# Kernel tuning notes

Measured on AMD Instinct MI355X. Metric: run time of the kernel, lower is better.

The kernel has to match this reference:

```python
import jax, jax.numpy as jnp
import numpy as np

B, N, K, C_IN, D = 4, 2048, 16, 480, 64
EPS = 1e-5


def _c1(x, w, b):
    # 1x1 Conv1d: x (B,C,N), w (O,C) -> (B,O,N)
    return jnp.einsum('oc,bcn->bon', w, x) + b[:, None]


def _c2(x, w, b):
    # 1x1 Conv2d: x (B,C,J,N), w (O,C) -> (B,O,J,N)
    return jnp.einsum('oc,bcjn->bojn', w, x) + b[:, None, None]


def _bn(x, g, b):
    # eval-mode BatchNorm2d with running_mean=0, running_var=1
    return x * (g / jnp.sqrt(1.0 + EPS))[:, None, None] + b[:, None, None]


def _mlp_res(x, w1, b1, w2, b2, ws, bs):
    return _c1(jax.nn.relu(_c1(x, w1, b1)), w2, b2) + _c1(x, ws, bs)


def _group(f, idx):
    # f (B,C,N), idx (B,K,N) int -> out[b,c,j,n] = f[b,c,idx[b,j,n]]  -> (B,C,K,N)
    return jax.vmap(lambda ff, ii: ff[:, ii])(f, idx)


def _knn_idx(xyz):
    # xyz (B,3,N) -> idx (B,K,N), excluding the self point (nearest neighbor)
    pts = xyz.transpose(0, 2, 1)  # (B,N,3)
    sq = jnp.sum(pts * pts, -1)
    d2 = sq[:, :, None] + sq[:, None, :] - 2.0 * jnp.einsum('bnd,bmd->bnm', pts, pts)
    _, idx = jax.lax.top_k(-d2, K + 1)  # (B,N,K+1), nearest first
    return idx.transpose(0, 2, 1)[:, 1:, :]  # drop self -> (B,K,N)


def _forward(idx, feature, xyz, bt1_w, bt1_b, bt2_w, bt2_b, bts_w, bts_b,
             q_w, q_b, k_w, k_b, v_w, v_b,
             fd1_w, fd1_b, fd_g, fd_bb, fd2_w, fd2_b,
             fg1_w, fg1_b, fg_g, fg_bb, fg2_w, fg2_b,
             at_w, at_b, m41_w, m41_b, m42_w, m42_b):
    x = _mlp_res(feature, bt1_w, bt1_b, bt2_w, bt2_b, bts_w, bts_b)  # (B,64,N)
    q = _c1(x, q_w, q_b)
    k = _c1(x, k_w, k_b)
    v = _c1(x, v_w, v_b)

    group_xyz = _group(xyz, idx)                       # (B,3,K,N)
    rel_xyz = xyz[:, :, None, :] - group_xyz           # (B,3,K,N)
    pos_enc = _c2(jax.nn.relu(_bn(_c2(rel_xyz, fd1_w, fd1_b), fd_g, fd_bb)), fd2_w, fd2_b)  # (B,64,K,N)

    k_local = _group(k, idx)                           # (B,64,K,N)
    v_local = _group(v, idx)
    qk_rel = q[:, :, None, :] - k_local
    attn = _c2(jax.nn.relu(_bn(_c2(qk_rel + pos_enc, fg1_w, fg1_b), fg_g, fg_bb)), fg2_w, fg2_b)  # (B,64,K,N)

    attn1 = attn.transpose(0, 1, 3, 2)                 # (B,64,N,K)
    # ConvTranspose2d(64,64,(4,1),(4,1)) with kernel==stride: out[b,o,4n+r,f] = sum_c x[b,c,n,f]*W[c,o,r] + bias[o]
    y = jnp.einsum('bcnf,cor->bonrf', attn1, at_w)
    y = y.reshape(y.shape[0], y.shape[1], -1, y.shape[4]) + at_b[None, :, None, None]  # (B,64,4N,K)
    attn = jax.nn.softmax(y, axis=1)

    value_rel = (v_local + pos_enc).transpose(0, 1, 3, 2)   # (B,64,N,K)
    value = jnp.repeat(value_rel, 4, axis=2)                # nearest upsample (4,1) -> (B,64,4N,K)

    res = jnp.einsum('bmnf,bmnf->bmn', attn, value)         # (B,64,4N)
    identity = jnp.repeat(x, 4, axis=2)                     # nearest upsample x4 -> (B,64,4N)
    res = res + identity
    completion = _c1(jax.nn.relu(_c1(res, m41_w, m41_b)), m42_w, m42_b)  # (B,3,4N)
    return completion, res


def setup_inputs() -> dict:
    key = jax.random.key(0)
    ks = jax.random.split(key, 24)
    i = iter(range(24))

    def w(shape):
        return (jax.random.normal(ks[next(i)], shape, dtype=jnp.float32) * 0.05)

    z = lambda n: jnp.zeros((n,), jnp.float32)
    o = lambda n: jnp.ones((n,), jnp.float32)
    return {
        'feature': jax.random.normal(ks[next(i)], (B, C_IN, N), dtype=jnp.float32),
        'xyz': jax.random.normal(ks[next(i)], (B, 3, N), dtype=jnp.float32),
        'bt1_w': w((D, C_IN)), 'bt1_b': z(D),
        'bt2_w': w((D, D)), 'bt2_b': z(D),
        'bts_w': w((D, C_IN)), 'bts_b': z(D),
        'q_w': w((D, D)), 'q_b': z(D),
        'k_w': w((D, D)), 'k_b': z(D),
        'v_w': w((D, D)), 'v_b': z(D),
        'fd1_w': w((D, 3)), 'fd1_b': z(D), 'fd_g': o(D), 'fd_bb': z(D),
        'fd2_w': w((D, D)), 'fd2_b': z(D),
        'fg1_w': w((4 * D, D)), 'fg1_b': z(4 * D), 'fg_g': o(4 * D), 'fg_bb': z(4 * D),
        'fg2_w': w((D, 4 * D)), 'fg2_b': z(D),
        'at_w': w((D, D, 4)), 'at_b': z(D),
        'm41_w': w((D, D)), 'm41_b': z(D),
        'm42_w': w((3, D)), 'm42_b': z(3),
    }


def reference(feature, xyz, bt1_w, bt1_b, bt2_w, bt2_b, bts_w, bts_b,
              q_w, q_b, k_w, k_b, v_w, v_b,
              fd1_w, fd1_b, fd_g, fd_bb, fd2_w, fd2_b,
              fg1_w, fg1_b, fg_g, fg_bb, fg2_w, fg2_b,
              at_w, at_b, m41_w, m41_b, m42_w, m42_b):
    idx = _knn_idx(xyz)
    return _forward(idx, feature, xyz, bt1_w, bt1_b, bt2_w, bt2_b, bts_w, bts_b,
                    q_w, q_b, k_w, k_b, v_w, v_b,
                    fd1_w, fd1_b, fd_g, fd_bb, fd2_w, fd2_b,
                    fg1_w, fg1_b, fg_g, fg_bb, fg2_w, fg2_b,
                    at_w, at_b, m41_w, m41_b, m42_w, m42_b)
```

## Files before the change

### kernel.cpp

```cpp
#include <hip/hip_runtime.h>

#define B_ 4
#define N_ 2048
#define K_ 16
#define CIN_ 480
#define UPN_ 8192
#define M_ (B_*N_*K_)
#define MX_ (B_*N_)
#define KCAP 448

typedef unsigned int u32;
typedef unsigned short u16;
typedef unsigned long long u64;
typedef __attribute__((ext_vector_type(8))) short short8;
typedef __attribute__((ext_vector_type(4))) float f32x4;

#define DEV static __device__ __forceinline__

DEV float b2f(u16 h){ return __uint_as_float(((u32)h)<<16); }
DEV u16 f2b(float f){
  u32 u = __float_as_uint(f);
  u32 r = u + 0x7fffu + ((u>>16)&1u);
  return (u16)(r>>16);
}
DEV u32 pack2(float a, float b){ return (u32)f2b(a) | ((u32)f2b(b)<<16); }
DEV bool detect_bf(const void* fg){ return ((((const u32*)fg)[0]) & 0xFFFFu) == 0x3F80u; }
DEV float ld(const void* p, int i, bool bf){
  return bf ? b2f(((const u16*)p)[i]) : ((const float*)p)[i];
}
DEV u64 makekey(float d2, int m){
  u32 bits = __float_as_uint(d2);
  bits = (bits & 0x80000000u) ? ~bits : (bits | 0x80000000u);
  return ((u64)bits<<32) | (u32)m;
}
DEV int swz64(int row, int colByte){ return row*128 + (colByte ^ ((row&7)<<4)); }
DEV int swzH (int row, int colByte){ return row*512 + (colByte ^ ((row&7)<<4)); }

__global__ __launch_bounds__(256) void convert_kernel(const void* __restrict__ xyz,
    const void* __restrict__ fg, float* __restrict__ fxyz)
{
  bool bf = detect_bf(fg);
  const int XT = B_*3*N_;
  for(int i = blockIdx.x*256+threadIdx.x; i < XT; i += gridDim.x*256)
    fxyz[i] = bf ? b2f(((const u16*)xyz)[i]) : ((const float*)xyz)[i];
}

__global__ __launch_bounds__(256) void transpose_kernel(const void* __restrict__ feature,
    const void* __restrict__ fg, u16* __restrict__ fxbT)
{
  __shared__ u16 s[32][34];
  bool bf = detect_bf(fg);
  int ntile = blockIdx.x, ctile = blockIdx.y, b = blockIdx.z;
  int tx = threadIdx.x & 31, ty = threadIdx.x >> 5;
  u64 base = (u64)b*CIN_*N_;
  #pragma unroll
  for(int r=0;r<4;r++){
    int c = ctile*32 + ty + r*8;
    int n = ntile*32 + tx;
    u64 i = base + (u64)c*N_ + n;
    s[ty + r*8][tx] = bf ? ((const u16*)feature)[i] : f2b(((const float*)feature)[i]);
  }
  __syncthreads();
  #pragma unroll
  for(int r=0;r<4;r++){
    int nl = ty + r*8;
    int n = ntile*32 + nl;
    fxbT[(u64)b*N_*CIN_ + (u64)n*CIN_ + ctile*32 + tx] = s[tx][nl];
  }
}

__global__ __launch_bounds__(256) void prep_kernel(
    const void* __restrict__ bt1_w, const void* __restrict__ bt1_b,
    const void* __restrict__ bt2_w, const void* __restrict__ bt2_b,
    const void* __restrict__ bts_w, const void* __restrict__ bts_b,
    const void* __restrict__ q_w, const void* __restrict__ q_b,
    const void* __restrict__ k_w, const void* __restrict__ k_b,
    const void* __restrict__ v_w, const void* __restrict__ v_b,
    const void* __restrict__ fd1_w, const void* __restrict__ fd1_b,
    const void* __restrict__ fd_g, const void* __restrict__ fd_bb,
    const void* __restrict__ fd2_w, const void* __restrict__ fd2_b,
    const void* __restrict__ fg1_w, const void* __restrict__ fg1_b,
    const void* __restrict__ fg_g, const void* __restrict__ fg_bb,
    const void* __restrict__ fg2_w, const void* __restrict__ fg2_b,
    const void* __restrict__ at_w, const void* __restrict__ at_b,
    const void* __restrict__ m41_w, const void* __restrict__ m41_b,
    const void* __restrict__ m42_w, const void* __restrict__ m42_b,
    float* __restrict__ W, u16* __restrict__ WB)
{
  int t = blockIdx.x*256 + threadIdx.x;
// ... 60 lines not shown
  __syncthreads();
  int w = threadIdx.x>>6, l = threadIdx.x&63;
  int q = blockIdx.x*4 + w;
  float qx=px[q], qy=py[q], qz=pz[q], qs=sq[q];
  float d2c[32];
  u64 best=~0ull;
  #pragma unroll
  for(int j=0;j<32;j++){
    int m = l*32 + ((j+l)&31);
    float d2 = (qs+sq[m]) - 2.0f*(qx*px[m]+qy*py[m]+qz*pz[m]);
    d2c[j]=d2;
    u64 key = makekey(d2, m);
    best = key<best ? key : best;
  }
  smin[w][l]=best;
  __syncthreads();
  {
    int rank=0;
    for(int i=0;i<64;i++) rank += (smin[w][i] < best);
    if(rank==16) stau[w] = best;
  }
  __syncthreads();
  u64 tau = stau[w];
  int myc=0;
  #pragma unroll
  for(int j=0;j<32;j++){
    int m = l*32 + ((j+l)&31);
    myc += (makekey(d2c[j], m) <= tau);
  }
  scnt[w][l]=myc;
  __syncthreads();
  int off=0, tot=0;
  for(int i=0;i<64;i++){
    int c = scnt[w][i];
    tot += c;
    off += (i<l) ? c : 0;
  }
  #pragma unroll
  for(int j=0;j<32;j++){
    int m = l*32 + ((j+l)&31);
    u64 key = makekey(d2c[j], m);
    if(key<=tau && off<KCAP){ sbuf[w][off]=key; off++; }
  }
  __syncthreads();
  if(tot>KCAP) tot=KCAP;
  for(int p=l; p<tot; p+=64){
    u64 kk = sbuf[w][p];
    int rk=0;
    for(int i=0;i<tot;i++) rk += (sbuf[w][i] < kk);
    if(rk>=1 && rk<17) idx[(b*K_+(rk-1))*N_+q] = ((int)(kk & 0xffffffffu)) & (N_-1);
  }
}

__global__ __launch_bounds__(256) void gemm480_mfma(const u16* __restrict__ A,
    const u16* __restrict__ Wt, const float* __restrict__ bias,
    u16* __restrict__ hout, float* __restrict__ xsout)
{
  int tid=threadIdx.x, w=tid>>6, lane=tid&63;
  int rbase=(blockIdx.x*4+w)*64;
  int cbase=blockIdx.y*64;
  int lr=lane&15, lk=(lane>>4)*8;
  f32x4 acc[4][4];
  #pragma unroll
  for(int i=0;i<4;i++)
    #pragma unroll
    for(int j=0;j<4;j++) acc[i][j]=(f32x4){0.f,0.f,0.f,0.f};
  for(int kc=0;kc<CIN_;kc+=32){
    short8 a[4], bb[4];
    #pragma unroll
    for(int ti=0;ti<4;ti++)
      a[ti] = *(const short8*)(A + (u64)(rbase+ti*16+lr)*CIN_ + kc + lk);
    #pragma unroll
    for(int tj=0;tj<4;tj++)
      bb[tj] = *(const short8*)(Wt + (u64)(cbase+tj*16+lr)*CIN_ + kc + lk);
    #pragma unroll
    for(int ti=0;ti<4;ti++)
      #pragma unroll
      for(int tj=0;tj<4;tj++)
        acc[ti][tj] = __builtin_amdgcn_mfma_f32_16x16x32_bf16(a[ti], bb[tj], acc[ti][tj], 0,0,0);
  }
  int rq=(lane>>4)*4;
  #pragma unroll
  for(int ti=0;ti<4;ti++)
    #pragma unroll
    for(int tj=0;tj<4;tj++){
      int col = cbase + tj*16 + lr;
      float bv = bias[col];
      #pragma unroll
      for(int reg=0;reg<4;reg++){
        u64 row = rbase + ti*16 + rq + reg;
        float vv = acc[ti][tj][reg] + bv;
        if(blockIdx.y==0) hout[row*64 + col] = f2b(fmaxf(vv,0.f));
        else              xsout[row*64 + (col-64)] = vv;
      }
    }
}

__global__ __launch_bounds__(256) void x_mfma(const u16* __restrict__ A,
    const u16* __restrict__ Wt, const float* __restrict__ bias,
    const float* __restrict__ xs, float* __restrict__ x, u16* __restrict__ xb)
{
  int tid=threadIdx.x, w=tid>>6, lane=tid&63;
  int rbase=(blockIdx.x*4+w)*64;
  int lr=lane&15, lk=(lane>>4)*8;
  f32x4 acc[4][4];
  #pragma unroll
  for(int i=0;i<4;i++)
    #pragma unroll
    for(int j=0;j<4;j++) acc[i][j]=(f32x4){0.f,0.f,0.f,0.f};
  for(int kc=0;kc<64;kc+=32){
    short8 a[4], bb[4];
    #pragma unroll
    for(int ti=0;ti<4;ti++)
      a[ti] = *(const short8*)(A + (u64)(rbase+ti*16+lr)*64 + kc + lk);
    #pragma unroll
    for(int tj=0;tj<4;tj++)
      bb[tj] = *(const short8*)(Wt + (u64)(tj*16+lr)*64 + kc + lk);
    #pragma unroll
    for(int ti=0;ti<4;ti++)
      #pragma unroll
      for(int tj=0;tj<4;tj++)
        acc[ti][tj] = __builtin_amdgcn_mfma_f32_16x16x32_bf16(a[ti], bb[tj], acc[ti][tj], 0,0,0);
  }
  int rq=(lane>>4)*4;
  #pragma unroll
  for(int ti=0;ti<4;ti++)
    #pragma unroll
    for(int tj=0;tj<4;tj++){
      int col = tj*16 + lr;
      float bv = bias[col];
      #pragma unroll
      for(int reg=0;reg<4;reg++){
        u64 row = rbase + ti*16 + rq + reg;
        float vv = acc[ti][tj][reg] + bv + xs[row*64+col];
        x[row*64+col] = vv;
        xb[row*64+col] = f2b(vv);
      }
    }
}

__global__ __launch_bounds__(256) void qkv_mfma(const u16* __restrict__ A,
    const u16* __restrict__ Wt, const float* __restrict__ bias, float* __restrict__ qkv)
{
  int tid=threadIdx.x, w=tid>>6, lane=tid&63;
  int rbase=(blockIdx.x*4+w)*64;
  int cbase=blockIdx.y*64;
  int lr=lane&15, lk=(lane>>4)*8;
  f32x4 acc[4][4];
  #pragma unroll
  for(int i=0;i<4;i++)
    #pragma unroll
    for(int j=0;j<4;j++) acc[i][j]=(f32x4){0.f,0.f,0.f,0.f};
  for(int kc=0;kc<64;kc+=32){
    short8 a[4], bb[4];
    #pragma unroll
    for(int ti=0;ti<4;ti++)
      a[ti] = *(const short8*)(A + (u64)(rbase+ti*16+lr)*64 + kc + lk);
    #pragma unroll
    for(int tj=0;tj<4;tj++)
      bb[tj] = *(const short8*)(Wt + (u64)(cbase+tj*16+lr)*64 + kc + lk);
    #pragma unroll
    for(int ti=0;ti<4;ti++)
      #pragma unroll
      for(int tj=0;tj<4;tj++)
        acc[ti][tj] = __builtin_amdgcn_mfma_f32_16x16x32_bf16(a[ti], bb[tj], acc[ti][tj], 0,0,0);
  }
  int rq=(lane>>4)*4;
  #pragma unroll
  for(int ti=0;ti<4;ti++)
    #pragma unroll
    for(int tj=0;tj<4;tj++){
      int col = cbase + tj*16 + lr;
      float bv = bias[col];
      #pragma unroll
      for(int reg=0;reg<4;reg++){
        u64 row = rbase + ti*16 + rq + reg;
        qkv[row*192 + col] = acc[ti][tj][reg] + bv;
      }
    }
}

__global__ __launch_bounds__(256) void fused_chain(
    const int* __restrict__ idx, const float* __restrict__ fxyz,
    const float* __restrict__ qkv, const float* __restrict__ x,
    const float* __restrict__ fd1f,
    const u16* __restrict__ Wfd2, const float* __restrict__ bfd2,
    const u16* __restrict__ Wfg1, const float* __restrict__ bfg1,
    const u16* __restrict__ Wfg2, const float* __restrict__ bfg2,
    const u16* __restrict__ Wat,  const float* __restrict__ bat,
    const void* __restrict__ det, void* __restrict__ out)
{
  __shared__ alignas(16) unsigned char lds[49152];
  int tid = threadIdx.x;
  int w = tid>>6, lane = tid&63;
  int lr = lane&15, lk = (lane>>4)*8, rq = (lane>>4)*4;

  int erow = tid>>2, ecg = tid&3;
  int el = erow>>4, ef = erow&15;
  int bn_e = blockIdx.x*4 + el;
  int b_e = bn_e>>11, n_e = bn_e&(N_-1);
  int jn = idx[(b_e*K_+ef)*N_ + n_e] & (N_-1);

  {
    const float* xb = fxyz + (u64)b_e*3*N_;
    float rx = xb[n_e]      - xb[jn];
    float ry = xb[N_+n_e]   - xb[N_+jn];
    float rz = xb[2*N_+n_e] - xb[2*N_+jn];
    #pragma unroll
    for(int gg=0; gg<4; gg++){
      u64 pk=0;
      #pragma unroll
      for(int j=0;j<4;j++){
        f32x4 wv = *(const f32x4*)(fd1f + ((ecg*4+gg)*4+j)*4);
        float tv = fmaxf(wv[0]*rx + wv[1]*ry + wv[2]*rz + wv[3], 0.f);
        pk |= (u64)f2b(tv) << (16*j);
      }
      *(u64*)(lds + swz64(erow, (ecg*4+gg)*8)) = pk;
    }
  }
  __syncthreads();

  {
    f32x4 acc[4];
    #pragma unroll
    for(int i=0;i<4;i++) acc[i]=(f32x4){0.f,0.f,0.f,0.f};
    #pragma unroll
    for(int kc=0;kc<64;kc+=32){
      short8 wf = *(const short8*)(Wfd2 + (u64)(w*16+lr)*64 + kc + lk);
      #pragma unroll
      for(int ti=0;ti<4;ti++){
        short8 tf = *(const short8*)(lds + swz64(ti*16+lr, (kc+lk)*2));
        acc[ti] = __builtin_amdgcn_mfma_f32_16x16x32_bf16(wf, tf, acc[ti], 0,0,0);
      }
    }
    f32x4 b4 = *(const f32x4*)(bfd2 + w*16 + rq);
    #pragma unroll
    for(int ti=0;ti<4;ti++){
      u64 pk=0;
      #pragma unroll
      for(int reg=0;reg<4;reg++) pk |= (u64)f2b(acc[ti][reg] + b4[reg]) << (16*reg);
      *(u64*)(lds + 8192 + swz64(ti*16+lr, (w*16+rq)*2)) = pk;
    }
  }
  __syncthreads();

  {
    int mg = ecg*16;
    const float* qrow = qkv + (u64)(b_e*N_+n_e)*192 + mg;
    const float* krow = qkv + (u64)(b_e*N_+jn)*192 + 64 + mg;
    const float* vrow = qkv + (u64)(b_e*N_+jn)*192 + 128 + mg;
    #pragma unroll
    for(int g2=0; g2<4; g2++){
      f32x4 qv = *(const f32x4*)(qrow + g2*4);
      f32x4 kv = *(const f32x4*)(krow + g2*4);
      f32x4 vv = *(const f32x4*)(vrow + g2*4);
      int cb = (mg + g2*4)*2;
      u64 pw = *(const u64*)(lds + 8192 + swz64(erow, cb));
      u64 aw=0, vw=0;
      #pragma unroll
      for(int j=0;j<4;j++){
        float pv = b2f((u16)(pw>>(16*j)));
        aw |= (u64)f2b(qv[j] - kv[j] + pv) << (16*j);
        vw |= (u64)f2b(vv[j] + pv) << (16*j);
      }
      *(u64*)(lds + swz64(erow, cb)) = aw;
      *(u64*)(lds + 8192 + swz64(erow, cb)) = vw;
    }
  }
  __syncthreads();

  {
    f32x4 acc[4][4];
    #pragma unroll
    for(int i=0;i<4;i++)
      #pragma unroll
      for(int j=0;j<4;j++) acc[i][j]=(f32x4){0.f,0.f,0.f,0.f};
    #pragma unroll
    for(int kc=0;kc<64;kc+=32){
      short8 wf[4], af[4];
      #pragma unroll
      for(int ti=0;ti<4;ti++)
        wf[ti] = *(const short8*)(Wfg1 + (u64)(w*64+ti*16+lr)*64 + kc + lk);
      #pragma unroll
      for(int tj=0;tj<4;tj++)
        af[tj] = *(const short8*)(lds + swz64(tj*16+lr, (kc+lk)*2));
      #pragma unroll
      for(int ti=0;ti<4;ti++)
        #pragma unroll
        for(int tj=0;tj<4;tj++)
          acc[ti][tj] = __builtin_amdgcn_mfma_f32_16x16x32_bf16(wf[ti], af[tj], acc[ti][tj], 0,0,0);
    }
    #pragma unroll
    for(int ti=0;ti<4;ti++){
      f32x4 b4 = *(const f32x4*)(bfg1 + w*64 + ti*16 + rq);
      #pragma unroll
      for(int tj=0;tj<4;tj++){
        int rowh = tj*16 + lr;
        u64 pk=0;
        #pragma unroll
        for(int reg=0;reg<4;reg++)
          pk |= (u64)f2b(fmaxf(acc[ti][tj][reg] + b4[reg], 0.f)) << (16*reg);
        *(u64*)(lds + 16384 + swzH(rowh, (w*64+ti*16+rq)*2)) = pk;
      }
    }
  }
  __syncthreads();

  {
    f32x4 acc[4];
    #pragma unroll
    for(int i=0;i<4;i++) acc[i]=(f32x4){0.f,0.f,0.f,0.f};
    #pragma unroll
    for(int kc=0;kc<256;kc+=32){
      short8 wf = *(const short8*)(Wfg2 + (u64)(w*16+lr)*256 + kc + lk);
      #pragma unroll
      for(int ti=0;ti<4;ti++){
        short8 hf = *(const short8*)(lds + 16384 + swzH(ti*16+lr, (kc+lk)*2));
        acc[ti] = __builtin_amdgcn_mfma_f32_16x16x32_bf16(wf, hf, acc[ti], 0,0,0);
      }
    }
    f32x4 b4 = *(const f32x4*)(bfg2 + w*16 + rq);
    #pragma unroll
    for(int ti=0;ti<4;ti++){
      u64 pk=0;
      #pragma unroll
      for(int reg=0;reg<4;reg++) pk |= (u64)f2b(acc[ti][reg] + b4[reg]) << (16*reg);
      *(u64*)(lds + swz64(ti*16+lr, (w*16+rq)*2)) = pk;
    }
  }
  __syncthreads();

  {
    f32x4 acc[4][4];
    #pragma unroll
    for(int i=0;i<4;i++)
      #pragma unroll
      for(int j=0;j<4;j++) acc[i][j]=(f32x4){0.f,0.f,0.f,0.f};
    #pragma unroll
    for(int kc=0;kc<64;kc+=32){
      short8 wf[4], gf[4];
      #pragma unroll
      for(int ti=0;ti<4;ti++)
        wf[ti] = *(const short8*)(Wat + (u64)(w*64+ti*16+lr)*64 + kc + lk);
      #pragma unroll
      for(int tj=0;tj<4;tj++)
        gf[tj] = *(const short8*)(lds + swz64(tj*16+lr, (kc+lk)*2));
      #pragma unroll
      for(int ti=0;ti<4;ti++)
        #pragma unroll
        for(int tj=0;tj<4;tj++)
          acc[ti][tj] = __builtin_amdgcn_mfma_f32_16x16x32_bf16(wf[ti], gf[tj], acc[ti][tj], 0,0,0);
    }
    #pragma unroll
    for(int ti=0;ti<4;ti++){
      f32x4 b4 = *(const f32x4*)(bat + w*64 + ti*16 + rq);
      #pragma unroll
      for(int tj=0;tj<4;tj++){
        int rowy = tj*16 + lr;
        u64 pk=0;
        #pragma unroll
        for(int reg=0;reg<4;reg++)
          pk |= (u64)f2b(acc[ti][tj][reg] + b4[reg]) << (16*reg);
        *(u64*)(lds + 16384 + swzH(rowy, (w*64+ti*16+rq)*2)) = pk;
      }
    }
  }
  __syncthreads();

  int f = lane>>2, r = lane&3;
  int rowl = w*16 + f;
  float yv[64];
  #pragma unroll
  for(int j=0;j<8;j++){
    uint4 pk = *(const uint4*)(lds + 16384 + swzH(rowl, r*128 + j*16));
    yv[j*8+0]=__uint_as_float(pk.x<<16); yv[j*8+1]=__uint_as_float(pk.x&0xffff0000u);
    yv[j*8+2]=__uint_as_float(pk.y<<16); yv[j*8+3]=__uint_as_float(pk.y&0xffff0000u);
    yv[j*8+4]=__uint_as_float(pk.z<<16); yv[j*8+5]=__uint_as_float(pk.z&0xffff0000u);
    yv[j*8+6]=__uint_as_float(pk.w<<16); yv[j*8+7]=__uint_as_float(pk.w&0xffff0000u);
  }
  __syncthreads();

  float mx = yv[0];
  #pragma unroll
  for(int m=1;m<64;m++) mx = fmaxf(mx, yv[m]);
  float sm = 0.f;
  #pragma unroll
  for(int m=0;m<64;m++){ float e = __expf(yv[m]-mx); yv[m]=e; sm+=e; }
  float rinv = 1.0f/sm;
  #pragma unroll
  for(int j=0;j<8;j++){
    uint4 pk;
    pk.x = pack2(yv[j*8+0]*rinv, yv[j*8+1]*rinv);
    pk.y = pack2(yv[j*8+2]*rinv, yv[j*8+3]*rinv);
    pk.z = pack2(yv[j*8+4]*rinv, yv[j*8+5]*rinv);
    pk.w = pack2(yv[j*8+6]*rinv, yv[j*8+7]*rinv);
    *(uint4*)(lds + 16384 + swz64(tid, j*16)) = pk;
  }
  __syncthreads();

  int m = lane;
  float a0=0.f,a1=0.f,a2=0.f,a3=0.f;
  #pragma unroll
  for(int f2=0; f2<16; f2++){
    float vvf = b2f(*(const u16*)(lds + 8192 + swz64(w*16+f2, m*2)));
    int spr = w*64 + f2*4;
    a0 += b2f(*(const u16*)(lds + 16384 + swz64(spr+0, m*2))) * vvf;
    a1 += b2f(*(const u16*)(lds + 16384 + swz64(spr+1, m*2))) * vvf;
    a2 += b2f(*(const u16*)(lds + 16384 + swz64(spr+2, m*2))) * vvf;
    a3 += b2f(*(const u16*)(lds + 16384 + swz64(spr+3, m*2))) * vvf;
  }
  int bn = blockIdx.x*4 + w;
  int b = bn>>11, n = bn&(N_-1);
  float xv = x[(u64)bn*64 + m];
  u64 off = 98304 + ((u64)(b*64+m))*UPN_ + (u64)n*4;
  if(detect_bf(det)){
    u64 pk = (u64)f2b(a0+xv) | ((u64)f2b(a1+xv)<<16)
           | ((u64)f2b(a2+xv)<<32) | ((u64)f2b(a3+xv)<<48);
    *(u64*)((u16*)out + off) = pk;
  } else {
    f32x4 pk = {a0+xv, a1+xv, a2+xv, a3+xv};
    *(f32x4*)((float*)out + off) = pk;
  }
}

__global__ __launch_bounds__(256) void comp_kernel(
  const float* __restrict__ m41T, const float* __restrict__ m41b,
  const float* __restrict__ m42f, const float* __restrict__ m42b,
  const void* __restrict__ det, void* __restrict__ out)
{
  int t = blockIdx.x*256 + threadIdx.x;
  int un = t & (UPN_-1);
  int b = t >> 13;
  bool bf = detect_bf(det);
  float acc[64];
  #pragma unroll
  for(int o=0;o<64;o++) acc[o] = m41b[o];
  if(bf){
    const u16* rr = (const u16*)out + 98304 + (u64)b*64*UPN_ + un;
    for(int c=0;c<64;c++){
      float rv = b2f(rr[(u64)c*UPN_]);
      const float* w = m41T + c*64;
      #pragma unroll
      for(int o=0;o<64;o++) acc[o] += w[o]*rv;
    }
  } else {
    const float* rr = (const float*)out + 98304 + (u64)b*64*UPN_ + un;
    for(int c=0;c<64;c++){
      float rv = rr[(u64)c*UPN_];
      const float* w = m41T + c*64;
      #pragma unroll
      for(int o=0;o<64;o++) acc[o] += w[o]*rv;
    }
  }
  float c0=m42b[0], c1=m42b[1], c2=m42b[2];
  #pragma unroll
  for(int o=0;o<64;o++){
    float hv = fmaxf(acc[o],0.f);
    c0 += m42f[o]*hv; c1 += m42f[64+o]*hv; c2 += m42f[128+o]*hv;
  }
  u64 base = (u64)b*3*UPN_ + un;
  if(bf){
    u16* cp = (u16*)out;
    cp[base]=f2b(c0); cp[base+UPN_]=f2b(c1); cp[base+2*UPN_]=f2b(c2);
  } else {
    float* cp = (float*)out;
    cp[base]=c0; cp[base+UPN_]=c1; cp[base+2*UPN_]=c2;
  }
}

extern "C" void kernel_launch(void* const* d_in, const int* in_sizes, int n_in,
                              void* d_out, int out_size, void* d_ws, size_t ws_size,
                              hipStream_t stream)
{
  (void)in_sizes; (void)n_in; (void)out_size; (void)ws_size;
  const void* feature=d_in[0];
  const void* xyz   =d_in[1];
  const void* bt1_w =d_in[2];  const void* bt1_b=d_in[3];
  const void* bt2_w =d_in[4];  const void* bt2_b=d_in[5];
  const void* bts_w =d_in[6];  const void* bts_b=d_in[7];
  const void* q_w   =d_in[8];  const void* q_b =d_in[9];
  const void* k_w   =d_in[10]; const void* k_b =d_in[11];
  const void* v_w   =d_in[12]; const void* v_b =d_in[13];
  const void* fd1_w =d_in[14]; const void* fd1_b=d_in[15];
  const void* fd_g  =d_in[16]; const void* fd_bb=d_in[17];
  const void* fd2_w =d_in[18]; const void* fd2_b=d_in[19];
  const void* fg1_w =d_in[20]; const void* fg1_b=d_in[21];
  const void* fg_g  =d_in[22]; const void* fg_bb=d_in[23];
  const void* fg2_w =d_in[24]; const void* fg2_b=d_in[25];
  const void* at_w  =d_in[26]; const void* at_b =d_in[27];
  const void* m41_w =d_in[28]; const void* m41_b=d_in[29];
  const void* m42_w =d_in[30]; const void* m42_b=d_in[31];

  char* ws=(char*)d_ws;
  float* W   =(float*)(ws);
  u16*  WB   =(u16*)  (ws + 589824);
  int*  idx  =(int*)  (ws + 851968);
  float* x   =(float*)(ws + 1376256);
  float* qkv =(float*)(ws + 3473408);
  u16*  h    =(u16*)  (ws + 9764864);
  float* xs  =(float*)(ws + 10813440);
  u16*  xb   =(u16*)  (ws + 12910592);
  u16*  fxbT =(u16*)  (ws + 114622464);
  float* fxyz=(float*)(ws + 122486784);

  const float* W_fd1f = W+77824;
  const float* W_fg1fb= W+98560;
  const float* W_m41T = W+131584;
  const float* W_m42  = W+135680;
  const float* Wb_g480= W+135872;
  const float* Wb_bt2 = W+136000;
  const float* Wb_qkv = W+136064;
  const float* Wb_fd2 = W+136256;
  const float* Wb_fg2 = W+136320;
  const float* Wb_m41 = W+136448;
  const float* Wb_m42 = W+136512;
  const float* W_atb256 = W+136576;
  const u16* WB_fg1  = WB;
  const u16* WB_fg2  = WB+16384;
  const u16* WB_at   = WB+32768;
  const u16* WB_fd2  = WB+49152;
  const u16* WB_g480 = WB+53248;
  const u16* WB_bt2  = WB+114688;
  const u16* WB_qkv  = WB+118784;

  convert_kernel<<<96,256,0,stream>>>(xyz, fd_g, fxyz);
  prep_kernel<<<1047,256,0,stream>>>(bt1_w,bt1_b,bt2_w,bt2_b,bts_w,bts_b,q_w,q_b,k_w,k_b,
      v_w,v_b,fd1_w,fd1_b,fd_g,fd_bb,fd2_w,fd2_b,fg1_w,fg1_b,fg_g,fg_bb,fg2_w,fg2_b,
      at_w,at_b,m41_w,m41_b,m42_w,m42_b,W,WB);
  transpose_kernel<<<dim3(64,15,4),256,0,stream>>>(feature, fd_g, fxbT);
  knn_kernel<<<dim3(N_/4,B_),256,0,stream>>>(fxyz, idx);
  gemm480_mfma<<<dim3(MX_/256,2),256,0,stream>>>(fxbT, WB_g480, Wb_g480, h, xs);
  x_mfma<<<MX_/256,256,0,stream>>>(h, WB_bt2, Wb_bt2, xs, x, xb);
  qkv_mfma<<<dim3(MX_/256,3),256,0,stream>>>(xb, WB_qkv, Wb_qkv, qkv);
  fused_chain<<<B_*N_/4,256,0,stream>>>(idx, fxyz, qkv, x, W_fd1f,
      WB_fd2, Wb_fd2, WB_fg1, W_fg1fb, WB_fg2, Wb_fg2, WB_at, W_atb256, fd_g, d_out);
  comp_kernel<<<128,256,0,stream>>>(W_m41T, Wb_m41, W_m42, Wb_m42, fd_g, d_out);
}
```

Measured before the change: 279.3 us.

## Fuse prefix GEMMs into one kernel and restructure attention chain with hardware bf16 packing

Merges the three prefix GEMM kernels (480-channel MLP, bt2 residual, qkv) into a single kernel that keeps intermediates in LDS, removing the round trips through global memory and two launches. The fused_chain kernel is reorganised: fg1/fg2 now run in two halves so less LDS is needed (48KB down to 32KB), and the transposed-conv, softmax and weighted-sum stage is processed one of the four output rows at a time, with shuffle reductions. Software bf16 rounding is replaced by the v_cvt_pk_bf16_f32 instruction. In exchange, the prefix kernel launches only 32 blocks with large register use, and the chain kernel has more barriers.

Measured after the change: 286.7 us. +2.6%, slower.

```diff
diff --git a/kernel.cpp b/kernel.cpp
--- a/kernel.cpp
+++ b/kernel.cpp
@@ -23,7 +23,13 @@
   u32 r = u + 0x7fffu + ((u>>16)&1u);
   return (u16)(r>>16);
 }
-DEV u32 pack2(float a, float b){ return (u32)f2b(a) | ((u32)f2b(b)<<16); }
+DEV u32 cvtpk(float a, float b){
+  u32 r; asm("v_cvt_pk_bf16_f32 %0, %1, %2" : "=v"(r) : "v"(a), "v"(b));
+  return r;
+}
+DEV u64 cvtpk4(float a, float b, float c, float d){
+  return (u64)cvtpk(a,b) | ((u64)cvtpk(c,d)<<32);
+}
 DEV bool detect_bf(const void* fg){ return ((((const u32*)fg)[0]) & 0xFFFFu) == 0x3F80u; }
 DEV float ld(const void* p, int i, bool bf){
   return bf ? b2f(((const u16*)p)[i]) : ((const float*)p)[i];
@@ -33,8 +39,8 @@
   bits = (bits & 0x80000000u) ? ~bits : (bits | 0x80000000u);
   return ((u64)bits<<32) | (u32)m;
 }
-DEV int swz64(int row, int colByte){ return row*128 + (colByte ^ ((row&7)<<4)); }
-DEV int swzH (int row, int colByte){ return row*512 + (colByte ^ ((row&7)<<4)); }
+DEV int swz64 (int row, int colByte){ return row*128 + (colByte ^ ((row&7)<<4)); }
+DEV int swz128(int row, int colByte){ return row*256 + (colByte ^ ((row&7)<<4)); }
 
 __global__ __launch_bounds__(256) void convert_kernel(const void* __restrict__ xyz,
     const void* __restrict__ fg, float* __restrict__ fxyz)
@@ -201,132 +207,127 @@
   }
 }
 
-__global__ __launch_bounds__(256) void gemm480_mfma(const u16* __restrict__ A,
-    const u16* __restrict__ Wt, const float* __restrict__ bias,
-    u16* __restrict__ hout, float* __restrict__ xsout)
-{
+__global__ __launch_bounds__(256,1) void prefix_mfma(const u16* __restrict__ A,
+    const u16* __restrict__ Wg, const float* __restrict__ bg,
+    const u16* __restrict__ Wbt2, const float* __restrict__ bbt2,
+    const u16* __restrict__ Wqkv, const float* __restrict__ bqkv,
+    float* __restrict__ x, float* __restrict__ qkvout)
+{
+  __shared__ alignas(16) unsigned char sh[65536];
   int tid=threadIdx.x, w=tid>>6, lane=tid&63;
-  int rbase=(blockIdx.x*4+w)*64;
-  int cbase=blockIdx.y*64;
-  int lr=lane&15, lk=(lane>>4)*8;
-  f32x4 acc[4][4];
+  int lr=lane&15, lk=(lane>>4)*8, rq=(lane>>4)*4;
+  u64 rbase=(u64)(blockIdx.x*4+w)*64;
+  int lrow0 = w*64;
+
+  f32x4 acc_h[4][4], acc_s[4][4];
   #pragma unroll
   for(int i=0;i<4;i++)
     #pragma unroll
-    for(int j=0;j<4;j++) acc[i][j]=(f32x4){0.f,0.f,0.f,0.f};
+    for(int j=0;j<4;j++){ acc_h[i][j]=(f32x4){0.f,0.f,0.f,0.f}; acc_s[i][j]=(f32x4){0.f,0.f,0.f,0.f}; }
   for(int kc=0;kc<CIN_;kc+=32){
-    short8 a[4], bb[4];
-    #pragma unroll
-    for(int ti=0;ti<4;ti++)
-      a[ti] = *(const short8*)(A + (u64)(rbase+ti*16+lr)*CIN_ + kc + lk);
-    #pragma unroll
-    for(int tj=0;tj<4;tj++)
-      bb[tj] = *(const short8*)(Wt + (u64)(cbase+tj*16+lr)*CIN_ + kc + lk);
-    #pragma unroll
-    for(int ti=0;ti<4;ti++)
-      #pragma unroll
-      for(int tj=0;tj<4;tj++)
-        acc[ti][tj] = __builtin_amdgcn_mfma_f32_16x16x32_bf16(a[ti], bb[tj], acc[ti][tj], 0,0,0);
-  }
-  int rq=(lane>>4)*4;
-  #pragma unroll
-  for(int ti=0;ti<4;ti++)
-    #pragma unroll
-    for(int tj=0;tj<4;tj++){
-      int col = cbase + tj*16 + lr;
-      float bv = bias[col];
-      #pragma unroll
-      for(int reg=0;reg<4;reg++){
-        u64 row = rbase + ti*16 + rq + reg;
-        float vv = acc[ti][tj][reg] + bv;
-        if(blockIdx.y==0) hout[row*64 + col] = f2b(fmaxf(vv,0.f));
-        else              xsout[row*64 + (col-64)] = vv;
-      }
-    }
-}
-
-__global__ __launch_bounds__(256) void x_mfma(const u16* __restrict__ A,
-    const u16* __restrict__ Wt, const float* __restrict__ bias,
-    const float* __restrict__ xs, float* __restrict__ x, u16* __restrict__ xb)
-{
-  int tid=threadIdx.x, w=tid>>6, lane=tid&63;
-  int rbase=(blockIdx.x*4+w)*64;
-  int lr=lane&15, lk=(lane>>4)*8;
-  f32x4 acc[4][4];
-  #pragma unroll
-  for(int i=0;i<4;i++)
-    #pragma unroll
-    for(int j=0;j<4;j++) acc[i][j]=(f32x4){0.f,0.f,0.f,0.f};
-  for(int kc=0;kc<64;kc+=32){
-    short8 a[4], bb[4];
-    #pragma unroll
-    for(int ti=0;ti<4;ti++)
-      a[ti] = *(const short8*)(A + (u64)(rbase+ti*16+lr)*64 + kc + lk);
-    #pragma unroll
-    for(int tj=0;tj<4;tj++)
-      bb[tj] = *(const short8*)(Wt + (u64)(tj*16+lr)*64 + kc + lk);
-    #pragma unroll
-    for(int ti=0;ti<4;ti++)
-      #pragma unroll
-      for(int tj=0;tj<4;tj++)
-        acc[ti][tj] = __builtin_amdgcn_mfma_f32_16x16x32_bf16(a[ti], bb[tj], acc[ti][tj], 0,0,0);
-  }
-  int rq=(lane>>4)*4;
-  #pragma unroll
-  for(int ti=0;ti<4;ti++)
-    #pragma unroll
-    for(int tj=0;tj<4;tj++){
-      int col = tj*16 + lr;
-      float bv = bias[col];
-      #pragma unroll
-      for(int reg=0;reg<4;reg++){
-        u64 row = rbase + ti*16 + rq + reg;
-        float vv = acc[ti][tj][reg] + bv + xs[row*64+col];
-        x[row*64+col] = vv;
-        xb[row*64+col] = f2b(vv);
-      }
-    }
-}
-
-__global__ __launch_bounds__(256) void qkv_mfma(const u16* __restrict__ A,
-    const u16* __restrict__ Wt, const float* __restrict__ bias, float* __restrict__ qkv)
-{
-  int tid=threadIdx.x, w=tid>>6, lane=tid&63;
-  int rbase=(blockIdx.x*4+w)*64;
-  int cbase=blockIdx.y*64;
-  int lr=lane&15, lk=(lane>>4)*8;
-  f32x4 acc[4][4];
-  #pragma unroll
-  for(int i=0;i<4;i++)
-    #pragma unroll
-    for(int j=0;j<4;j++) acc[i][j]=(f32x4){0.f,0.f,0.f,0.f};
-  for(int kc=0;kc<64;kc+=32){
-    short8 a[4], bb[4];
-    #pragma unroll
-    for(int ti=0;ti<4;ti++)
-      a[ti] = *(const short8*)(A + (u64)(rbase+ti*16+lr)*64 + kc + lk);
-    #pragma unroll
-    for(int tj=0;tj<4;tj++)
-      bb[tj] = *(const short8*)(Wt + (u64)(cbase+tj*16+lr)*64 + kc + lk);
-    #pragma unroll
-    for(int ti=0;ti<4;ti++)
-      #pragma unroll
-      for(int tj=0;tj<4;tj++)
-        acc[ti][tj] = __builtin_amdgcn_mfma_f32_16x16x32_bf16(a[ti], bb[tj], acc[ti][tj], 0,0,0);
-  }
-  int rq=(lane>>4)*4;
-  #pragma unroll
-  for(int ti=0;ti<4;ti++)
-    #pragma unroll
-    for(int tj=0;tj<4;tj++){
-      int col = cbase + tj*16 + lr;
-      float bv = bias[col];
-      #pragma unroll
-      for(int reg=0;reg<4;reg++){
-        u64 row = rbase + ti*16 + rq + reg;
-        qkv[row*192 + col] = acc[ti][tj][reg] + bv;
-      }
-    }
+    short8 af[4], wh[4], ws[4];
+    #pragma unroll
+    for(int ta=0;ta<4;ta++)
+      af[ta] = *(const short8*)(A + (rbase+ta*16+lr)*CIN_ + kc + lk);
+    #pragma unroll
+    for(int tw=0;tw<4;tw++){
+      wh[tw] = *(const short8*)(Wg + (u64)(tw*16+lr)*CIN_ + kc + lk);
+      ws[tw] = *(const short8*)(Wg + (u64)(64+tw*16+lr)*CIN_ + kc + lk);
+    }
+    #pragma unroll
+    for(int tw=0;tw<4;tw++)
+      #pragma unroll
+      for(int ta=0;ta<4;ta++){
+        acc_h[tw][ta] = __builtin_amdgcn_mfma_f32_16x16x32_bf16(wh[tw], af[ta], acc_h[tw][ta], 0,0,0);
+        acc_s[tw][ta] = __builtin_amdgcn_mfma_f32_16x16x32_bf16(ws[tw], af[ta], acc_s[tw][ta], 0,0,0);
+      }
+  }
+  #pragma unroll
+  for(int tw=0;tw<4;tw++){
+    f32x4 b4 = *(const f32x4*)(bg + tw*16 + rq);
+    #pragma unroll
+    for(int ta=0;ta<4;ta++){
+      int row = lrow0 + ta*16 + lr;
+      *(u64*)(sh + swz64(row, (tw*16+rq)*2)) =
+        cvtpk4(fmaxf(acc_h[tw][ta][0]+b4[0],0.f), fmaxf(acc_h[tw][ta][1]+b4[1],0.f),
+               fmaxf(acc_h[tw][ta][2]+b4[2],0.f), fmaxf(acc_h[tw][ta][3]+b4[3],0.f));
+    }
+  }
+  __syncthreads();
+  {
+    f32x4 acc_x[4][4];
+    #pragma unroll
+    for(int i=0;i<4;i++)
+      #pragma unroll
+      for(int j=0;j<4;j++) acc_x[i][j]=(f32x4){0.f,0.f,0.f,0.f};
+    #pragma unroll
+    for(int kc=0;kc<64;kc+=32){
+      short8 wf[4], hf[4];
+      #pragma unroll
+      for(int tw=0;tw<4;tw++)
+        wf[tw] = *(const short8*)(Wbt2 + (u64)(tw*16+lr)*64 + kc + lk);
+      #pragma unroll
+      for(int ta=0;ta<4;ta++)
+        hf[ta] = *(const short8*)(sh + swz64(lrow0+ta*16+lr, (kc+lk)*2));
+      #pragma unroll
+      for(int tw=0;tw<4;tw++)
+        #pragma unroll
+        for(int ta=0;ta<4;ta++)
+          acc_x[tw][ta] = __builtin_amdgcn_mfma_f32_16x16x32_bf16(wf[tw], hf[ta], acc_x[tw][ta], 0,0,0);
+    }
+    #pragma unroll
+    for(int tw=0;tw<4;tw++){
+      f32x4 bb = *(const f32x4*)(bbt2 + tw*16 + rq);
+      f32x4 bs = *(const f32x4*)(bg + 64 + tw*16 + rq);
+      #pragma unroll
+      for(int ta=0;ta<4;ta++){
+        int row = lrow0 + ta*16 + lr;
+        f32x4 xv;
+        #pragma unroll
+        for(int reg=0;reg<4;reg++){
+          float xsv = acc_s[tw][ta][reg] + bs[reg];
+          xv[reg] = acc_x[tw][ta][reg] + bb[reg] + xsv;
+        }
+        *(f32x4*)(x + (rbase+ta*16+lr)*64 + tw*16 + rq) = xv;
+        *(u64*)(sh + 32768 + swz64(row, (tw*16+rq)*2)) = cvtpk4(xv[0],xv[1],xv[2],xv[3]);
+      }
+    }
+  }
+  __syncthreads();
+  #pragma unroll
+  for(int g=0;g<3;g++){
+    f32x4 acc[4][4];
+    #pragma unroll
+    for(int i=0;i<4;i++)
+      #pragma unroll
+      for(int j=0;j<4;j++) acc[i][j]=(f32x4){0.f,0.f,0.f,0.f};
+    #pragma unroll
+    for(int kc=0;kc<64;kc+=32){
+      short8 wf[4], hf[4];
+      #pragma unroll
+      for(int tw=0;tw<4;tw++)
+        wf[tw] = *(const short8*)(Wqkv + (u64)(g*64+tw*16+lr)*64 + kc + lk);
+      #pragma unroll
+      for(int ta=0;ta<4;ta++)
+        hf[ta] = *(const short8*)(sh + 32768 + swz64(lrow0+ta*16+lr, (kc+lk)*2));
+      #pragma unroll
+      for(int tw=0;tw<4;tw++)
+        #pragma unroll
+        for(int ta=0;ta<4;ta++)
+          acc[tw][ta] = __builtin_amdgcn_mfma_f32_16x16x32_bf16(wf[tw], hf[ta], acc[tw][ta], 0,0,0);
+    }
+    #pragma unroll
+    for(int tw=0;tw<4;tw++){
+      f32x4 bq = *(const f32x4*)(bqkv + g*64 + tw*16 + rq);
+      #pragma unroll
+      for(int ta=0;ta<4;ta++){
+        f32x4 ov;
+        #pragma unroll
+        for(int reg=0;reg<4;reg++) ov[reg] = acc[tw][ta][reg] + bq[reg];
+        *(f32x4*)(qkvout + (rbase+ta*16+lr)*192 + g*64 + tw*16 + rq) = ov;
+      }
+    }
+  }
 }
 
 __global__ __launch_bounds__(256) void fused_chain(
@@ -339,7 +340,7 @@
     const u16* __restrict__ Wat,  const float* __restrict__ bat,
     const void* __restrict__ det, void* __restrict__ out)
 {
-  __shared__ alignas(16) unsigned char lds[49152];
+  __shared__ alignas(16) unsigned char lds[32768];
   int tid = threadIdx.x;
   int w = tid>>6, lane = tid&63;
   int lr = lane&15, lk = (lane>>4)*8, rq = (lane>>4)*4;
@@ -357,14 +358,13 @@
     float rz = xb[2*N_+n_e] - xb[2*N_+jn];
     #pragma unroll
     for(int gg=0; gg<4; gg++){
-      u64 pk=0;
+      float tv[4];
       #pragma unroll
       for(int j=0;j<4;j++){
         f32x4 wv = *(const f32x4*)(fd1f + ((ecg*4+gg)*4+j)*4);
-        float tv = fmaxf(wv[0]*rx + wv[1]*ry + wv[2]*rz + wv[3], 0.f);
-        pk |= (u64)f2b(tv) << (16*j);
-      }
-      *(u64*)(lds + swz64(erow, (ecg*4+gg)*8)) = pk;
+        tv[j] = fmaxf(wv[0]*rx + wv[1]*ry + wv[2]*rz + wv[3], 0.f);
+      }
+      *(u64*)(lds + swz64(erow, (ecg*4+gg)*8)) = cvtpk4(tv[0],tv[1],tv[2],tv[3]);
     }
   }
   __syncthreads();
@@ -384,12 +384,9 @@
     }
     f32x4 b4 = *(const f32x4*)(bfd2 + w*16 + rq);
     #pragma unroll
-    for(int ti=0;ti<4;ti++){
-      u64 pk=0;
-      #pragma unroll
-      for(int reg=0;reg<4;reg++) pk |= (u64)f2b(acc[ti][reg] + b4[reg]) << (16*reg);
-      *(u64*)(lds + 8192 + swz64(ti*16+lr, (w*16+rq)*2)) = pk;
-    }
+    for(int ti=0;ti<4;ti++)
+      *(u64*)(lds + 8192 + swz64(ti*16+lr, (w*16+rq)*2)) =
+        cvtpk4(acc[ti][0]+b4[0], acc[ti][1]+b4[1], acc[ti][2]+b4[2], acc[ti][3]+b4[3]);
   }
   __syncthreads();
 
@@ -405,169 +402,153 @@
       f32x4 vv = *(const f32x4*)(vrow + g2*4);
       int cb = (mg + g2*4)*2;
       u64 pw = *(const u64*)(lds + 8192 + swz64(erow, cb));
-      u64 aw=0, vw=0;
-      #pragma unroll
-      for(int j=0;j<4;j++){
-        float pv = b2f((u16)(pw>>(16*j)));
-        aw |= (u64)f2b(qv[j] - kv[j] + pv) << (16*j);
-        vw |= (u64)f2b(vv[j] + pv) << (16*j);
-      }
-      *(u64*)(lds + swz64(erow, cb)) = aw;
-      *(u64*)(lds + 8192 + swz64(erow, cb)) = vw;
-    }
-  }
-  __syncthreads();
+      float p0=b2f((u16)pw), p1=b2f((u16)(pw>>16)), p2=b2f((u16)(pw>>32)), p3=b2f((u16)(pw>>48));
+      *(u64*)(lds + swz64(erow, cb)) =
+        cvtpk4(qv[0]-kv[0]+p0, qv[1]-kv[1]+p1, qv[2]-kv[2]+p2, qv[3]-kv[3]+p3);
+      *(u64*)(lds + 8192 + swz64(erow, cb)) =
+        cvtpk4(vv[0]+p0, vv[1]+p1, vv[2]+p2, vv[3]+p3);
+    }
+  }
+  __syncthreads();
+
+  float vreg[16];
+  #pragma unroll
+  for(int f2=0; f2<16; f2++)
+    vreg[f2] = b2f(*(const u16*)(lds + 8192 + swz64(w*16+f2, lane*2)));
+
+  f32x4 gacc[4];
+  #pragma unroll
+  for(int i=0;i<4;i++) gacc[i]=(f32x4){0.f,0.f,0.f,0.f};
+  #pragma unroll
+  for(int half=0; half<2; half++){
+    {
+      f32x4 hacc[2][4];
+      #pragma unroll
+      for(int i=0;i<2;i++)
+        #pragma unroll
+        for(int j=0;j<4;j++) hacc[i][j]=(f32x4){0.f,0.f,0.f,0.f};
+      #pragma unroll
+      for(int kc=0;kc<64;kc+=32){
+        short8 wf[2], af[4];
+        #pragma unroll
+        for(int ti=0;ti<2;ti++)
+          wf[ti] = *(const short8*)(Wfg1 + (u64)(half*128 + w*32 + ti*16 + lr)*64 + kc + lk);
+        #pragma unroll
+        for(int tj=0;tj<4;tj++)
+          af[tj] = *(const short8*)(lds + swz64(tj*16+lr, (kc+lk)*2));
+        #pragma unroll
+        for(int ti=0;ti<2;ti++)
+          #pragma unroll
+          for(int tj=0;tj<4;tj++)
+            hacc[ti][tj] = __builtin_amdgcn_mfma_f32_16x16x32_bf16(wf[ti], af[tj], hacc[ti][tj], 0,0,0);
+      }
+      #pragma unroll
+      for(int ti=0;ti<2;ti++){
+        f32x4 b4 = *(const f32x4*)(bfg1 + half*128 + w*32 + ti*16 + rq);
+        #pragma unroll
+        for(int tj=0;tj<4;tj++){
+          int row = tj*16 + lr;
+          *(u64*)(lds + 16384 + swz128(row, (w*32+ti*16+rq)*2)) =
+            cvtpk4(fmaxf(hacc[ti][tj][0]+b4[0],0.f), fmaxf(hacc[ti][tj][1]+b4[1],0.f),
+                   fmaxf(hacc[ti][tj][2]+b4[2],0.f), fmaxf(hacc[ti][tj][3]+b4[3],0.f));
+        }
+      }
+    }
+    __syncthreads();
+    #pragma unroll
+    for(int kc=0;kc<128;kc+=32){
+      short8 wf = *(const short8*)(Wfg2 + (u64)(w*16+lr)*256 + half*128 + kc + lk);
+      #pragma unroll
+      for(int tj=0;tj<4;tj++){
+        short8 hf = *(const short8*)(lds + 16384 + swz128(tj*16+lr, (kc+lk)*2));
+        gacc[tj] = __builtin_amdgcn_mfma_f32_16x16x32_bf16(wf, hf, gacc[tj], 0,0,0);
+      }
+    }
+    __syncthreads();
+  }
 
   {
-    f32x4 acc[4][4];
-    #pragma unroll
-    for(int i=0;i<4;i++)
-      #pragma unroll
-      for(int j=0;j<4;j++) acc[i][j]=(f32x4){0.f,0.f,0.f,0.f};
-    #pragma unroll
-    for(int kc=0;kc<64;kc+=32){
-      short8 wf[4], af[4];
-      #pragma unroll
-      for(int ti=0;ti<4;ti++)
-        wf[ti] = *(const short8*)(Wfg1 + (u64)(w*64+ti*16+lr)*64 + kc + lk);
+    f32x4 b4 = *(const f32x4*)(bfg2 + w*16 + rq);
+    #pragma unroll
+    for(int tj=0;tj<4;tj++)
+      *(u64*)(lds + swz64(tj*16+lr, (w*16+rq)*2)) =
+        cvtpk4(gacc[tj][0]+b4[0], gacc[tj][1]+b4[1], gacc[tj][2]+b4[2], gacc[tj][3]+b4[3]);
+  }
+  __syncthreads();
+
+  float aout[4];
+  int srow = tid>>2, sub = tid&3;
+  #pragma unroll
+  for(int r=0;r<4;r++){
+    {
+      f32x4 acc[4];
+      #pragma unroll
+      for(int i=0;i<4;i++) acc[i]=(f32x4){0.f,0.f,0.f,0.f};
+      #pragma unroll
+      for(int kc=0;kc<64;kc+=32){
+        short8 wf = *(const short8*)(Wat + (u64)(r*64 + w*16 + lr)*64 + kc + lk);
+        #pragma unroll
+        for(int tj=0;tj<4;tj++){
+          short8 gf = *(const short8*)(lds + swz64(tj*16+lr, (kc+lk)*2));
+          acc[tj] = __builtin_amdgcn_mfma_f32_16x16x32_bf16(wf, gf, acc[tj], 0,0,0);
+        }
+      }
+      f32x4 b4 = *(const f32x4*)(bat + r*64 + w*16 + rq);
       #pragma unroll
       for(int tj=0;tj<4;tj++)
-        af[tj] = *(const short8*)(lds + swz64(tj*16+lr, (kc+lk)*2));
-      #pragma unroll
-      for(int ti=0;ti<4;ti++)
-        #pragma unroll
-        for(int tj=0;tj<4;tj++)
-          acc[ti][tj] = __builtin_amdgcn_mfma_f32_16x16x32_bf16(wf[ti], af[tj], acc[ti][tj], 0,0,0);
-    }
-    #pragma unroll
-    for(int ti=0;ti<4;ti++){
-      f32x4 b4 = *(const f32x4*)(bfg1 + w*64 + ti*16 + rq);
-      #pragma unroll
-      for(int tj=0;tj<4;tj++){
-        int rowh = tj*16 + lr;
-        u64 pk=0;
-        #pragma unroll
-        for(int reg=0;reg<4;reg++)
-          pk |= (u64)f2b(fmaxf(acc[ti][tj][reg] + b4[reg], 0.f)) << (16*reg);
-        *(u64*)(lds + 16384 + swzH(rowh, (w*64+ti*16+rq)*2)) = pk;
-      }
-    }
-  }
-  __syncthreads();
-
-  {
-    f32x4 acc[4];
-    #pragma unroll
-    for(int i=0;i<4;i++) acc[i]=(f32x4){0.f,0.f,0.f,0.f};
-    #pragma unroll
-    for(int kc=0;kc<256;kc+=32){
-      short8 wf = *(const short8*)(Wfg2 + (u64)(w*16+lr)*256 + kc + lk);
-      #pragma unroll
-      for(int ti=0;ti<4;ti++){
-        short8 hf = *(const short8*)(lds + 16384 + swzH(ti*16+lr, (kc+lk)*2));
-        acc[ti] = __builtin_amdgcn_mfma_f32_16x16x32_bf16(wf, hf, acc[ti], 0,0,0);
-      }
-    }
-    f32x4 b4 = *(const f32x4*)(bfg2 + w*16 + rq);
-    #pragma unroll
-    for(int ti=0;ti<4;ti++){
-      u64 pk=0;
-      #pragma unroll
-      for(int reg=0;reg<4;reg++) pk |= (u64)f2b(acc[ti][reg] + b4[reg]) << (16*reg);
-      *(u64*)(lds + swz64(ti*16+lr, (w*16+rq)*2)) = pk;
-    }
-  }
-  __syncthreads();
-
-  {
-    f32x4 acc[4][4];
-    #pragma unroll
-    for(int i=0;i<4;i++)
-      #pragma unroll
-      for(int j=0;j<4;j++) acc[i][j]=(f32x4){0.f,0.f,0.f,0.f};
-    #pragma unroll
-    for(int kc=0;kc<64;kc+=32){
-      short8 wf[4], gf[4];
-      #pragma unroll
-      for(int ti=0;ti<4;ti++)
-        wf[ti] = *(const short8*)(Wat + (u64)(w*64+ti*16+lr)*64 + kc + lk);
-      #pragma unroll
-      for(int tj=0;tj<4;tj++)
-        gf[tj] = *(const short8*)(lds + swz64(tj*16+lr, (kc+lk)*2));
-      #pragma unroll
-      for(int ti=0;ti<4;ti++)
-        #pragma unroll
-        for(int tj=0;tj<4;tj++)
-          acc[ti][tj] = __builtin_amdgcn_mfma_f32_16x16x32_bf16(wf[ti], gf[tj], acc[ti][tj], 0,0,0);
-    }
-    #pragma unroll
-    for(int ti=0;ti<4;ti++){
-      f32x4 b4 = *(const f32x4*)(bat + w*64 + ti*16 + rq);
-      #pragma unroll
-      for(int tj=0;tj<4;tj++){
-        int rowy = tj*16 + lr;
-        u64 pk=0;
-        #pragma unroll
-        for(int reg=0;reg<4;reg++)
-          pk |= (u64)f2b(acc[ti][tj][reg] + b4[reg]) << (16*reg);
-        *(u64*)(lds + 16384 + swzH(rowy, (w*64+ti*16+rq)*2)) = pk;
-      }
-    }
-  }
-  __syncthreads();
-
-  int f = lane>>2, r = lane&3;
-  int rowl = w*16 + f;
-  float yv[64];
-  #pragma unroll
-  for(int j=0;j<8;j++){
-    uint4 pk = *(const uint4*)(lds + 16384 + swzH(rowl, r*128 + j*16));
-    yv[j*8+0]=__uint_as_float(pk.x<<16); yv[j*8+1]=__uint_as_float(pk.x&0xffff0000u);
-    yv[j*8+2]=__uint_as_float(pk.y<<16); yv[j*8+3]=__uint_as_float(pk.y&0xffff0000u);
-    yv[j*8+4]=__uint_as_float(pk.z<<16); yv[j*8+5]=__uint_as_float(pk.z&0xffff0000u);
-    yv[j*8+6]=__uint_as_float(pk.w<<16); yv[j*8+7]=__uint_as_float(pk.w&0xffff0000u);
-  }
-  __syncthreads();
-
-  float mx = yv[0];
-  #pragma unroll
-  for(int m=1;m<64;m++) mx = fmaxf(mx, yv[m]);
-  float sm = 0.f;
-  #pragma unroll
-  for(int m=0;m<64;m++){ float e = __expf(yv[m]-mx); yv[m]=e; sm+=e; }
-  float rinv = 1.0f/sm;
-  #pragma unroll
-  for(int j=0;j<8;j++){
-    uint4 pk;
-    pk.x = pack2(yv[j*8+0]*rinv, yv[j*8+1]*rinv);
-    pk.y = pack2(yv[j*8+2]*rinv, yv[j*8+3]*rinv);
-    pk.z = pack2(yv[j*8+4]*rinv, yv[j*8+5]*rinv);
-    pk.w = pack2(yv[j*8+6]*rinv, yv[j*8+7]*rinv);
-    *(uint4*)(lds + 16384 + swz64(tid, j*16)) = pk;
-  }
-  __syncthreads();
-
-  int m = lane;
-  float a0=0.f,a1=0.f,a2=0.f,a3=0.f;
-  #pragma unroll
-  for(int f2=0; f2<16; f2++){
-    float vvf = b2f(*(const u16*)(lds + 8192 + swz64(w*16+f2, m*2)));
-    int spr = w*64 + f2*4;
-    a0 += b2f(*(const u16*)(lds + 16384 + swz64(spr+0, m*2))) * vvf;
-    a1 += b2f(*(const u16*)(lds + 16384 + swz64(spr+1, m*2))) * vvf;
-    a2 += b2f(*(const u16*)(lds + 16384 + swz64(spr+2, m*2))) * vvf;
-    a3 += b2f(*(const u16*)(lds + 16384 + swz64(spr+3, m*2))) * vvf;
-  }
+        *(u64*)(lds + 16384 + swz64(tj*16+lr, (w*16+rq)*2)) =
+          cvtpk4(acc[tj][0]+b4[0], acc[tj][1]+b4[1], acc[tj][2]+b4[2], acc[tj][3]+b4[3]);
+    }
+    __syncthreads();
+    {
+      float yv[16];
+      uint4 pk0 = *(const uint4*)(lds + 16384 + swz64(srow, sub*32));
+      uint4 pk1 = *(const uint4*)(lds + 16384 + swz64(srow, sub*32 + 16));
+      yv[0]=__uint_as_float(pk0.x<<16); yv[1]=__uint_as_float(pk0.x&0xffff0000u);
+      yv[2]=__uint_as_float(pk0.y<<16); yv[3]=__uint_as_float(pk0.y&0xffff0000u);
+      yv[4]=__uint_as_float(pk0.z<<16); yv[5]=__uint_as_float(pk0.z&0xffff0000u);
+      yv[6]=__uint_as_float(pk0.w<<16); yv[7]=__uint_as_float(pk0.w&0xffff0000u);
+      yv[8]=__uint_as_float(pk1.x<<16); yv[9]=__uint_as_float(pk1.x&0xffff0000u);
+      yv[10]=__uint_as_float(pk1.y<<16); yv[11]=__uint_as_float(pk1.y&0xffff0000u);
+      yv[12]=__uint_as_float(pk1.z<<16); yv[13]=__uint_as_float(pk1.z&0xffff0000u);
+      yv[14]=__uint_as_float(pk1.w<<16); yv[15]=__uint_as_float(pk1.w&0xffff0000u);
+      float mx = yv[0];
+      #pragma unroll
+      for(int m=1;m<16;m++) mx = fmaxf(mx, yv[m]);
+      mx = fmaxf(mx, __shfl_xor(mx, 1));
+      mx = fmaxf(mx, __shfl_xor(mx, 2));
+      float sm = 0.f;
+      #pragma unroll
+      for(int m=0;m<16;m++){ float e = __expf(yv[m]-mx); yv[m]=e; sm+=e; }
+      sm += __shfl_xor(sm, 1);
+      sm += __shfl_xor(sm, 2);
+      float rinv = 1.0f/sm;
+      uint4 o0, o1;
+      o0.x = cvtpk(yv[0]*rinv, yv[1]*rinv);  o0.y = cvtpk(yv[2]*rinv, yv[3]*rinv);
+      o0.z = cvtpk(yv[4]*rinv, yv[5]*rinv);  o0.w = cvtpk(yv[6]*rinv, yv[7]*rinv);
+      o1.x = cvtpk(yv[8]*rinv, yv[9]*rinv);  o1.y = cvtpk(yv[10]*rinv, yv[11]*rinv);
+      o1.z = cvtpk(yv[12]*rinv, yv[13]*rinv); o1.w = cvtpk(yv[14]*rinv, yv[15]*rinv);
+      *(uint4*)(lds + 8192 + swz64(srow, sub*32))      = o0;
+      *(uint4*)(lds + 8192 + swz64(srow, sub*32 + 16)) = o1;
+    }
+    __syncthreads();
+    {
+      float a = 0.f;
+      #pragma unroll
+      for(int f2=0; f2<16; f2++)
+        a += b2f(*(const u16*)(lds + 8192 + swz64(w*16+f2, lane*2))) * vreg[f2];
+      aout[r] = a;
+    }
+  }
+
   int bn = blockIdx.x*4 + w;
   int b = bn>>11, n = bn&(N_-1);
-  float xv = x[(u64)bn*64 + m];
-  u64 off = 98304 + ((u64)(b*64+m))*UPN_ + (u64)n*4;
+  float xv = x[(u64)bn*64 + lane];
+  u64 off = 98304 + ((u64)(b*64+lane))*UPN_ + (u64)n*4;
   if(detect_bf(det)){
-    u64 pk = (u64)f2b(a0+xv) | ((u64)f2b(a1+xv)<<16)
-           | ((u64)f2b(a2+xv)<<32) | ((u64)f2b(a3+xv)<<48);
-    *(u64*)((u16*)out + off) = pk;
+    *(u64*)((u16*)out + off) = cvtpk4(aout[0]+xv, aout[1]+xv, aout[2]+xv, aout[3]+xv);
   } else {
-    f32x4 pk = {a0+xv, a1+xv, a2+xv, a3+xv};
+    f32x4 pk = {aout[0]+xv, aout[1]+xv, aout[2]+xv, aout[3]+xv};
     *(f32x4*)((float*)out + off) = pk;
   }
 }
@@ -646,9 +627,6 @@
   int*  idx  =(int*)  (ws + 851968);
   float* x   =(float*)(ws + 1376256);
   float* qkv =(float*)(ws + 3473408);
-  u16*  h    =(u16*)  (ws + 9764864);
-  float* xs  =(float*)(ws + 10813440);
-  u16*  xb   =(u16*)  (ws + 12910592);
   u16*  fxbT =(u16*)  (ws + 114622464);
   float* fxyz=(float*)(ws + 122486784);
 
@@ -678,9 +656,8 @@
       at_w,at_b,m41_w,m41_b,m42_w,m42_b,W,WB);
   transpose_kernel<<<dim3(64,15,4),256,0,stream>>>(feature, fd_g, fxbT);
   knn_kernel<<<dim3(N_/4,B_),256,0,stream>>>(fxyz, idx);
-  gemm480_mfma<<<dim3(MX_/256,2),256,0,stream>>>(fxbT, WB_g480, Wb_g480, h, xs);
-  x_mfma<<<MX_/256,256,0,stream>>>(h, WB_bt2, Wb_bt2, xs, x, xb);
-  qkv_mfma<<<dim3(MX_/256,3),256,0,stream>>>(xb, WB_qkv, Wb_qkv, qkv);
+  prefix_mfma<<<MX_/256,256,0,stream>>>(fxbT, WB_g480, Wb_g480,
+      WB_bt2, Wb_bt2, WB_qkv, Wb_qkv, x, qkv);
   fused_chain<<<B_*N_/4,256,0,stream>>>(idx, fxyz, qkv, x, W_fd1f,
       WB_fd2, Wb_fd2, WB_fg1, W_fg1fb, WB_fg2, Wb_fg2, WB_at, W_atb256, fd_g, d_out);
   comp_kernel<<<128,256,0,stream>>>(W_m41T, Wb_m41, W_m42, Wb_m42, fd_g, d_out);
```
